# Optimization experiments

Hardware: AMD Instinct MI355X
Metric: run time of the kernel (lower is better)

## Reference

```python
import jax, jax.numpy as jnp
import numpy as np

N = 2048   # graph nodes
K = 3      # Chebyshev order of LSTM cell graph conv
IN = 2     # input feature dim (in/out flow)
H = 64     # hidden dim
B = 16     # batch
T = 12     # encoder sequence length


def _cheb(L, x, order):
    """Chebyshev polynomial features. x: [B, N, F] -> [B, N, order*F]."""
    Tk = [x]
    if order > 1:
        Tk.append(jnp.einsum('nm,bmf->bnf', L, x))
    for _ in range(2, order):
        Tk.append(2.0 * jnp.einsum('nm,bmf->bnf', L, Tk[-1]) - Tk[-2])
    return jnp.concatenate(Tk, axis=-1)


def _cell(L, x, h, c, W, b):
    """Graph-conv LSTM cell. x: [B,N,IN], h/c: [B,N,H]."""
    comb = jnp.concatenate([x, h], axis=-1)          # [B, N, IN+H]
    gates = _cheb(L, comb, K) @ W + b                # [B, N, 4H]
    i, f, o, g = jnp.split(gates, 4, axis=-1)
    c2 = jax.nn.sigmoid(f) * c + jax.nn.sigmoid(i) * jnp.tanh(g)
    h2 = jax.nn.sigmoid(o) * jnp.tanh(c2)
    return h2, c2


def setup_inputs() -> dict:
    rng = np.random.default_rng(0)
    # random sparse symmetric adjacency (avg degree ~8) -> normalized Laplacian
    A = rng.random((N, N)) < 8.0 / N
    A = np.triu(A, 1)
    A = (A | A.T).astype(np.float32)
    d = np.clip(A.sum(1), 1.0, None)
    dinv = 1.0 / np.sqrt(d)
    Lap = (np.eye(N, dtype=np.float32) - dinv[:, None] * A * dinv[None, :]).astype(np.float32)

    key = jax.random.key(0)
    k1, k2, k3 = jax.random.split(key, 3)
    return {
        'input_tensor': jax.random.normal(k1, (B, T, N, IN), jnp.float32),
        'L': jnp.asarray(Lap),
        'W_cell': jax.random.normal(k2, (K * (IN + H), 4 * H), jnp.float32) * 0.05,
        'b_cell': jnp.zeros((4 * H,), jnp.float32),
        'W0': jax.random.normal(k3, (H, IN), jnp.float32) * 0.05,
        'b0': jnp.zeros((IN,), jnp.float32),
        'future': 12,
    }


def reference(input_tensor, L, W_cell, b_cell, W0, b0, future):
    bsz = input_tensor.shape[0]
    h0 = jnp.zeros((bsz, N, H), input_tensor.dtype)
    c0 = jnp.zeros((bsz, N, H), input_tensor.dtype)

    # encoder: unroll ConvLSTM over the input sequence
    def enc_step(carry, xt):
        h, c = carry
        h, c = _cell(L, xt, h, c, W_cell, b_cell)
        return (h, c), None

    (h, c), _ = jax.lax.scan(enc_step, (h0, c0), jnp.swapaxes(input_tensor, 0, 1))

    # conv0 has K=1 => per-node linear; first prediction from last hidden state
    x = jnp.tanh(h @ W0 + b0)                         # [B, N, IN]

    def dec_step(carry, _):
        h, c, x = carry
        h, c = _cell(L, x, h, c, W_cell, b_cell)
        x2 = jnp.tanh(h @ W0 + b0)
        return (h, c, x2), x2

    _, xs = jax.lax.scan(dec_step, (h, c, x), None, length=future - 1)
    if future > 1:
        out = jnp.concatenate([x[:, None], jnp.swapaxes(xs, 0, 1)], axis=1)
    else:
        out = x[:, None]
    return out  # [B, future, N, IN]
```

## Files before the change

### kernel.cpp

```cpp
#include <hip/hip_runtime.h>
#include <cstdint>
#include <cstddef>

#define NN   2048
#define BB   16
#define TT   12
#define FUT  12
#define HH   64
#define GG   256
#define KP   224
#define ELLW 72
#define ASTR 232
#define NODE_F 80

typedef __attribute__((ext_vector_type(8))) short bf16x8;
typedef __attribute__((ext_vector_type(4))) float f32x4;

__device__ __forceinline__ float sigmoidf_(float x) {
    return 1.f / (1.f + __expf(-x));
}
__device__ __forceinline__ float tanhf_(float x) {
    const float e = __expf(2.f * x);
    return 1.f - 2.f / (e + 1.f);
}
__device__ __forceinline__ unsigned short f2bf(float x) {
    unsigned u = __builtin_bit_cast(unsigned, x);
    u += 0x7fffu + ((u >> 16) & 1u);
    return (unsigned short)(u >> 16);
}
__device__ __forceinline__ float bf2f(unsigned short s) {
    unsigned u = ((unsigned)s) << 16;
    return __builtin_bit_cast(float, u);
}

__global__ __launch_bounds__(256) void build_ell(
    const float* __restrict__ L, int* __restrict__ cols,
    float* __restrict__ vals, int* __restrict__ cnt)
{
    const int n = blockIdx.x;
    const int t = threadIdx.x;
    const float* row = L + (size_t)n * NN;
    float v[8];
    int c = 0;
#pragma unroll
    for (int i = 0; i < 8; ++i) {
        v[i] = row[t * 8 + i];
        c += (v[i] != 0.f);
    }
    __shared__ int s[256];
    s[t] = c;
    __syncthreads();
    for (int d = 1; d < 256; d <<= 1) {
        int add = (t >= d) ? s[t - d] : 0;
        __syncthreads();
        s[t] += add;
        __syncthreads();
    }
    int o = s[t] - c;
#pragma unroll
    for (int i = 0; i < 8; ++i) {
        if (v[i] != 0.f) {
            if (o < ELLW) {
                cols[n * ELLW + o] = t * 8 + i;
                vals[n * ELLW + o] = v[i];
            }
            ++o;
        }
    }
    if (t == 255) {
        int cn = (s[255] < ELLW) ? s[255] : ELLW;
        int cn4 = (cn + 3) & ~3;
        if (cn4 > ELLW) cn4 = ELLW;
        for (int p = cn; p < cn4; ++p) {
            cols[n * ELLW + p] = n;
            vals[n * ELLW + p] = 0.f;
        }
        cnt[n] = cn4;
    }
}

__global__ __launch_bounds__(256) void wt_prep(
    const float* __restrict__ W, short* __restrict__ Wh, short* __restrict__ Wl)
{
    const int col = blockIdx.x;
    const int k = threadIdx.x;
    if (k < KP) {
        const float x = (k < 198) ? W[(size_t)k * GG + col] : 0.f;
        const unsigned short h = f2bf(x);
        const unsigned short l = f2bf(x - bf2f(h));
        Wh[(size_t)col * KP + k] = (short)h;
        Wl[(size_t)col * KP + k] = (short)l;
    }
}

__global__ __launch_bounds__(256) void x_trans(
    const float* __restrict__ input, float* __restrict__ xt)
{
    const int o = blockIdx.x * 256 + threadIdx.x;
    const int e = o & 1;
    const int b = (o >> 1) & 15;
    const int n = (o >> 5) & (NN - 1);
    const int t = o >> 16;
    xt[o] = input[(((size_t)b * TT + t) * NN + n) * 2 + e];
}

__global__ __launch_bounds__(256) void spmm_t1(
    const float* __restrict__ xt,
    const float* __restrict__ h,
    const int* __restrict__ cols, const float* __restrict__ vals,
    const int* __restrict__ cnt, float* __restrict__ t1)
{
    const int w = threadIdx.x >> 6, lane = threadIdx.x & 63;
    const int b = lane >> 2, j = lane & 3;
    const int n = blockIdx.x;
    const int cn = cnt[n];
    const int* cp = cols + n * ELLW;
    const float* vp = vals + n * ELLW;
    const int qoff = (4 * w + j) * 4;
    float a0 = 0.f, a1 = 0.f, a2 = 0.f, a3 = 0.f;
    float ax0 = 0.f, ax1 = 0.f;
#pragma unroll 4
    for (int jj = 0; jj < cn; ++jj) {
        const int m = cp[jj];
        const float v = vp[jj];
        const float4 g = *(const float4*)&h[((size_t)m * 16 + b) * HH + qoff];
        a0 += v * g.x; a1 += v * g.y; a2 += v * g.z; a3 += v * g.w;
        if (w == 0) {
            const float2 xg = *(const float2*)&xt[((size_t)m * 16 + b) * 2];
            ax0 += v * xg.x; ax1 += v * xg.y;
        }
    }
    float* o = t1 + ((size_t)n * 16 + b) * NODE_F;
    *(float4*)&o[qoff] = (float4){a0, a1, a2, a3};
    if (w == 0 && j == 0) {
        o[64] = ax0;
        o[65] = ax1;
    }
}

__global__ __launch_bounds__(256, 5) void cell_fused(
    const float* __restrict__ xt,
    float* __restrict__ h, float* __restrict__ c,
    const float* __restrict__ t1g,
    const int* __restrict__ cols, const float* __restrict__ vals,
    const int* __restrict__ cnt,
    const short* __restrict__ Wh, const short* __restrict__ Wl,
    const float* __restrict__ bc,
    const float* __restrict__ W0, const float* __restrict__ b0,
    float* __restrict__ xout,
    float* __restrict__ out, int jslot)
{
    __shared__ unsigned short Ah[32][ASTR];
    __shared__ unsigned short Al[32][ASTR];
    __shared__ float proj[4][32][2];
    const int tid = threadIdx.x, w = tid >> 6, lane = tid & 63;
    const int q = lane >> 4, c16 = lane & 15;
    const int b = lane >> 2, j = lane & 3;
    const int n0 = blockIdx.x * 2;
    const int qoff = (4 * w + j) * 4;

    auto put = [&](int r, int k, float v) {
        const unsigned short hi = f2bf(v);
        Ah[r][k] = hi;
        Al[r][k] = f2bf(v - bf2f(hi));
    };

    {
        const int zr = tid >> 3, zs = tid & 7;
#pragma unroll
        for (int k0 = 198; k0 < 232; k0 += 8) {
            const int k = k0 + zs;
            if (k < 232) { Ah[zr][k] = 0; Al[zr][k] = 0; }
        }
    }

#pragma unroll
    for (int ln = 0; ln < 2; ++ln) {
        const int n = n0 + ln;
        const size_t rb = (size_t)n * 16 + b;
        const int r = ln * 16 + b;
        const float4 hq = *(const float4*)&h[rb * HH + qoff];
        const float4 tq = *(const float4*)&t1g[rb * NODE_F + qoff];
        float xo0 = 0.f, xo1 = 0.f, t160 = 0.f, t161 = 0.f;
        if (w == 1) {
            const float2 xv = *(const float2*)&xt[rb * 2];
            xo0 = xv.x; xo1 = xv.y;
            const float2 tv = *(const float2*)&t1g[rb * NODE_F + 64];
            t160 = tv.x; t161 = tv.y;
        }
        const int cn = cnt[n];
        const int* cp = cols + n * ELLW;
        const float* vp = vals + n * ELLW;
        float a0 = 0.f, a1 = 0.f, a2 = 0.f, a3 = 0.f, ax0 = 0.f, ax1 = 0.f;
#pragma unroll 4
        for (int jj = 0; jj < cn; ++jj) {
            const int m = cp[jj];
            const float v = vp[jj];
            const size_t mb = ((size_t)m * 16 + b) * NODE_F;
            const float4 g = *(const float4*)&t1g[mb + qoff];
            a0 += v * g.x; a1 += v * g.y; a2 += v * g.z; a3 += v * g.w;
            if (w == 1) {
                const float2 gx = *(const float2*)&t1g[mb + 64];
                ax0 += v * gx.x; ax1 += v * gx.y;
            }
        }
        put(r, 2 + qoff + 0, hq.x);  put(r, 2 + qoff + 1, hq.y);
        put(r, 2 + qoff + 2, hq.z);  put(r, 2 + qoff + 3, hq.w);
        put(r, 68 + qoff + 0, tq.x); put(r, 68 + qoff + 1, tq.y);
        put(r, 68 + qoff + 2, tq.z); put(r, 68 + qoff + 3, tq.w);
        put(r, 134 + qoff + 0, 2.f * a0 - hq.x);
        put(r, 134 + qoff + 1, 2.f * a1 - hq.y);
        put(r, 134 + qoff + 2, 2.f * a2 - hq.z);
        put(r, 134 + qoff + 3, 2.f * a3 - hq.w);
        if (w == 1 && j == 0) {
            put(r, 0, xo0);  put(r, 1, xo1);
            put(r, 66, t160); put(r, 67, t161);
            put(r, 132, 2.f * ax0 - xo0);
            put(r, 133, 2.f * ax1 - xo1);
        }
    }
    __syncthreads();

    f32x4 acc[2][4];
#pragma unroll
    for (int rt = 0; rt < 2; ++rt)
#pragma unroll
        for (int g = 0; g < 4; ++g) acc[rt][g] = (f32x4){0.f, 0.f, 0.f, 0.f};

    const int wc = w;
#pragma unroll 1
    for (int kc = 0; kc < 7; ++kc) {
        const int ko = kc * 32 + q * 8;
        bf16x8 ah[2], al[2];
#pragma unroll
        for (int rt = 0; rt < 2; ++rt) {
            ah[rt] = *(const bf16x8*)&Ah[rt * 16 + c16][ko];
            al[rt] = *(const bf16x8*)&Al[rt * 16 + c16][ko];
        }
        bf16x8 bh[4], bl[4];
#pragma unroll
        for (int g = 0; g < 4; ++g) {
            const int col = (wc + 4 * g) * 16 + c16;
            const size_t wo = (size_t)col * KP + ko;
            bh[g] = *(const bf16x8*)(Wh + wo);
            bl[g] = *(const bf16x8*)(Wl + wo);
        }
#pragma unroll
        for (int rt = 0; rt < 2; ++rt)
#pragma unroll
            for (int g = 0; g < 4; ++g) {
                acc[rt][g] = __builtin_amdgcn_mfma_f32_16x16x32_bf16(ah[rt], bh[g], acc[rt][g], 0, 0, 0);
                acc[rt][g] = __builtin_amdgcn_mfma_f32_16x16x32_bf16(al[rt], bh[g], acc[rt][g], 0, 0, 0);
                acc[rt][g] = __builtin_amdgcn_mfma_f32_16x16x32_bf16(ah[rt], bl[g], acc[rt][g], 0, 0, 0);
            }
    }

    const int u = 16 * wc + c16;
    const float bi = bc[u], bfv = bc[64 + u], bo = bc[128 + u], bg = bc[192 + u];
    float h2v[2][4];
#pragma unroll
    for (int rt = 0; rt < 2; ++rt) {
        const int n = n0 + rt;
#pragma unroll
        for (int reg = 0; reg < 4; ++reg) {
            const int bb = q * 4 + reg;
            const size_t idx = ((size_t)n * 16 + bb) * HH + u;
            const float ig = sigmoidf_(acc[rt][0][reg] + bi);
            const float fg = sigmoidf_(acc[rt][1][reg] + bfv);
            const float og = sigmoidf_(acc[rt][2][reg] + bo);
            const float gg = tanhf_(acc[rt][3][reg] + bg);
            const float c2 = fg * c[idx] + ig * gg;
            const float h2 = og * tanhf_(c2);
            c[idx] = c2;
            h[idx] = h2;
            h2v[rt][reg] = h2;
        }
    }

    if (jslot >= 0) {
        const float w0u = W0[u * 2], w1u = W0[u * 2 + 1];
#pragma unroll
        for (int rt = 0; rt < 2; ++rt) {
#pragma unroll
            for (int reg = 0; reg < 4; ++reg) {
                float s0 = h2v[rt][reg] * w0u;
                float s1 = h2v[rt][reg] * w1u;
#pragma unroll
                for (int d = 1; d <= 8; d <<= 1) {
                    s0 += __shfl_xor(s0, d, 64);
                    s1 += __shfl_xor(s1, d, 64);
                }
                if (c16 == 0) {
                    const int lr = rt * 16 + q * 4 + reg;
                    proj[wc][lr][0] = s0;
                    proj[wc][lr][1] = s1;
                }
            }
        }
        __syncthreads();
        if (tid < 64) {
            const int lr = tid >> 1, comp = tid & 1;
            const float v = proj[0][lr][comp] + proj[1][lr][comp] +
                            proj[2][lr][comp] + proj[3][lr][comp] + b0[comp];
            const float y = tanhf_(v);
            const int n = n0 + (lr >> 4);
            const int bb = lr & 15;
            xout[((size_t)n * 16 + bb) * 2 + comp] = y;
            out[(((size_t)bb * FUT + jslot) * NN + n) * 2 + comp] = y;
        }
    }
}

extern "C" void kernel_launch(void* const* d_in, const int* in_sizes, int n_in,
                              void* d_out, int out_size, void* d_ws, size_t ws_size,
                              hipStream_t stream)
{
    const float* input = (const float*)d_in[0];
    const float* L     = (const float*)d_in[1];
    const float* W     = (const float*)d_in[2];
    const float* bc    = (const float*)d_in[3];
    const float* W0    = (const float*)d_in[4];
    const float* b0    = (const float*)d_in[5];

    char* ws = (char*)d_ws;
    size_t off = 0;
    auto carve = [&](size_t bytes) {
        void* p = ws + off;
        off += (bytes + 255) & ~(size_t)255;
        return p;
    };
    int*   cols  = (int*)  carve((size_t)NN * ELLW * 4);
    float* vals  = (float*)carve((size_t)NN * ELLW * 4);
    int*   cnt   = (int*)  carve((size_t)NN * 4);
    float* t1    = (float*)carve((size_t)NN * 16 * NODE_F * 4);
    float* h     = (float*)carve((size_t)NN * 16 * HH * 4);
    float* c     = (float*)carve((size_t)NN * 16 * HH * 4);
    float* xbuf  = (float*)carve((size_t)NN * 16 * 2 * 4);
    float* xtall = (float*)carve((size_t)TT * NN * 16 * 2 * 4);
    short* Wh    = (short*)carve((size_t)GG * KP * 2);
    short* Wl    = (short*)carve((size_t)GG * KP * 2);
    float* out   = (float*)d_out;

    build_ell<<<NN, 256, 0, stream>>>(L, cols, vals, cnt);
    wt_prep<<<GG, 256, 0, stream>>>(W, Wh, Wl);
    x_trans<<<(TT * NN * 16 * 2) / 256, 256, 0, stream>>>(input, xtall);
    hipMemsetAsync(h, 0, (size_t)NN * 16 * HH * 4, stream);
    hipMemsetAsync(c, 0, (size_t)NN * 16 * HH * 4, stream);

    for (int t = 0; t < TT; ++t) {
        const float* xt = xtall + (size_t)t * NN * 16 * 2;
        spmm_t1<<<NN, 256, 0, stream>>>(xt, h, cols, vals, cnt, t1);
        cell_fused<<<NN / 2, 256, 0, stream>>>(xt, h, c, t1, cols, vals, cnt,
                                               Wh, Wl, bc, W0, b0, xbuf, out,
                                               (t == TT - 1) ? 0 : -1);
    }
    for (int jstep = 1; jstep < FUT; ++jstep) {
        spmm_t1<<<NN, 256, 0, stream>>>(xbuf, h, cols, vals, cnt, t1);
        cell_fused<<<NN / 2, 256, 0, stream>>>(xbuf, h, c, t1, cols, vals, cnt,
                                               Wh, Wl, bc, W0, b0, xbuf, out, jstep);
    }
}
```

Measured before the change: 1.260 ms.

## Split Chebyshev T1 buffer into h/x arrays and process one node per block

The first-order Chebyshev term is now stored as a dense 64-wide hidden array plus a separate 2-wide input array, replacing the padded 80-float interleaved rows. This aligns the neighbour gathers. The fused cell kernel now handles a single node per block, with half the LDS and accumulators and a higher occupancy hint, and launches twice as many blocks. In exchange, each block reloads the full split-bf16 weight tile for only 16 rows, which doubles weight fetch traffic through the caches.

```diff
diff --git a/kernel.cpp b/kernel.cpp
--- a/kernel.cpp
+++ b/kernel.cpp
@@ -11,7 +11,6 @@
 #define KP   224
 #define ELLW 72
 #define ASTR 232
-#define NODE_F 80
 
 typedef __attribute__((ext_vector_type(8))) short bf16x8;
 typedef __attribute__((ext_vector_type(4))) float f32x4;
@@ -108,7 +107,8 @@
     const float* __restrict__ xt,
     const float* __restrict__ h,
     const int* __restrict__ cols, const float* __restrict__ vals,
-    const int* __restrict__ cnt, float* __restrict__ t1)
+    const int* __restrict__ cnt,
+    float* __restrict__ t1h, float* __restrict__ t1x)
 {
     const int w = threadIdx.x >> 6, lane = threadIdx.x & 63;
     const int b = lane >> 2, j = lane & 3;
@@ -130,18 +130,18 @@
             ax0 += v * xg.x; ax1 += v * xg.y;
         }
     }
-    float* o = t1 + ((size_t)n * 16 + b) * NODE_F;
-    *(float4*)&o[qoff] = (float4){a0, a1, a2, a3};
+    *(float4*)&t1h[((size_t)n * 16 + b) * HH + qoff] = (float4){a0, a1, a2, a3};
     if (w == 0 && j == 0) {
-        o[64] = ax0;
-        o[65] = ax1;
-    }
-}
-
-__global__ __launch_bounds__(256, 5) void cell_fused(
+        t1x[((size_t)n * 16 + b) * 2]     = ax0;
+        t1x[((size_t)n * 16 + b) * 2 + 1] = ax1;
+    }
+}
+
+__global__ __launch_bounds__(256, 8) void cell_fused(
     const float* __restrict__ xt,
     float* __restrict__ h, float* __restrict__ c,
-    const float* __restrict__ t1g,
+    const float* __restrict__ t1h,
+    const float* __restrict__ t1x,
     const int* __restrict__ cols, const float* __restrict__ vals,
     const int* __restrict__ cnt,
     const short* __restrict__ Wh, const short* __restrict__ Wl,
@@ -150,13 +150,13 @@
     float* __restrict__ xout,
     float* __restrict__ out, int jslot)
 {
-    __shared__ unsigned short Ah[32][ASTR];
-    __shared__ unsigned short Al[32][ASTR];
-    __shared__ float proj[4][32][2];
+    __shared__ unsigned short Ah[16][ASTR];
+    __shared__ unsigned short Al[16][ASTR];
+    __shared__ float proj[4][16][2];
     const int tid = threadIdx.x, w = tid >> 6, lane = tid & 63;
     const int q = lane >> 4, c16 = lane & 15;
     const int b = lane >> 2, j = lane & 3;
-    const int n0 = blockIdx.x * 2;
+    const int n = blockIdx.x;
     const int qoff = (4 * w + j) * 4;
 
     auto put = [&](int r, int k, float v) {
@@ -166,26 +166,23 @@
     };
 
     {
-        const int zr = tid >> 3, zs = tid & 7;
-#pragma unroll
-        for (int k0 = 198; k0 < 232; k0 += 8) {
+        const int zr = tid >> 4, zs = tid & 15;
+#pragma unroll
+        for (int k0 = 198; k0 < 232; k0 += 16) {
             const int k = k0 + zs;
             if (k < 232) { Ah[zr][k] = 0; Al[zr][k] = 0; }
         }
     }
 
-#pragma unroll
-    for (int ln = 0; ln < 2; ++ln) {
-        const int n = n0 + ln;
+    {
         const size_t rb = (size_t)n * 16 + b;
-        const int r = ln * 16 + b;
         const float4 hq = *(const float4*)&h[rb * HH + qoff];
-        const float4 tq = *(const float4*)&t1g[rb * NODE_F + qoff];
+        const float4 tq = *(const float4*)&t1h[rb * HH + qoff];
         float xo0 = 0.f, xo1 = 0.f, t160 = 0.f, t161 = 0.f;
         if (w == 1) {
             const float2 xv = *(const float2*)&xt[rb * 2];
             xo0 = xv.x; xo1 = xv.y;
-            const float2 tv = *(const float2*)&t1g[rb * NODE_F + 64];
+            const float2 tv = *(const float2*)&t1x[rb * 2];
             t160 = tv.x; t161 = tv.y;
         }
         const int cn = cnt[n];
@@ -196,14 +193,15 @@
         for (int jj = 0; jj < cn; ++jj) {
             const int m = cp[jj];
             const float v = vp[jj];
-            const size_t mb = ((size_t)m * 16 + b) * NODE_F;
-            const float4 g = *(const float4*)&t1g[mb + qoff];
+            const size_t mb = (size_t)m * 16 + b;
+            const float4 g = *(const float4*)&t1h[mb * HH + qoff];
             a0 += v * g.x; a1 += v * g.y; a2 += v * g.z; a3 += v * g.w;
             if (w == 1) {
-                const float2 gx = *(const float2*)&t1g[mb + 64];
+                const float2 gx = *(const float2*)&t1x[mb * 2];
                 ax0 += v * gx.x; ax1 += v * gx.y;
             }
         }
+        const int r = b;
         put(r, 2 + qoff + 0, hq.x);  put(r, 2 + qoff + 1, hq.y);
         put(r, 2 + qoff + 2, hq.z);  put(r, 2 + qoff + 3, hq.w);
         put(r, 68 + qoff + 0, tq.x); put(r, 68 + qoff + 1, tq.y);
@@ -213,7 +211,7 @@
         put(r, 134 + qoff + 2, 2.f * a2 - hq.z);
         put(r, 134 + qoff + 3, 2.f * a3 - hq.w);
         if (w == 1 && j == 0) {
-            put(r, 0, xo0);  put(r, 1, xo1);
+            put(r, 0, xo0);   put(r, 1, xo1);
             put(r, 66, t160); put(r, 67, t161);
             put(r, 132, 2.f * ax0 - xo0);
             put(r, 133, 2.f * ax1 - xo1);
@@ -221,92 +219,75 @@
     }
     __syncthreads();
 
-    f32x4 acc[2][4];
-#pragma unroll
-    for (int rt = 0; rt < 2; ++rt)
-#pragma unroll
-        for (int g = 0; g < 4; ++g) acc[rt][g] = (f32x4){0.f, 0.f, 0.f, 0.f};
-
-    const int wc = w;
+    f32x4 acc[4];
+#pragma unroll
+    for (int g = 0; g < 4; ++g) acc[g] = (f32x4){0.f, 0.f, 0.f, 0.f};
+
 #pragma unroll 1
     for (int kc = 0; kc < 7; ++kc) {
         const int ko = kc * 32 + q * 8;
-        bf16x8 ah[2], al[2];
-#pragma unroll
-        for (int rt = 0; rt < 2; ++rt) {
-            ah[rt] = *(const bf16x8*)&Ah[rt * 16 + c16][ko];
-            al[rt] = *(const bf16x8*)&Al[rt * 16 + c16][ko];
-        }
-        bf16x8 bh[4], bl[4];
-#pragma unroll
-        for (int g = 0; g < 4; ++g) {
-            const int col = (wc + 4 * g) * 16 + c16;
-            const size_t wo = (size_t)col * KP + ko;
-            bh[g] = *(const bf16x8*)(Wh + wo);
-            bl[g] = *(const bf16x8*)(Wl + wo);
-        }
-#pragma unroll
-        for (int rt = 0; rt < 2; ++rt)
-#pragma unroll
-            for (int g = 0; g < 4; ++g) {
-                acc[rt][g] = __builtin_amdgcn_mfma_f32_16x16x32_bf16(ah[rt], bh[g], acc[rt][g], 0, 0, 0);
-                acc[rt][g] = __builtin_amdgcn_mfma_f32_16x16x32_bf16(al[rt], bh[g], acc[rt][g], 0, 0, 0);
-                acc[rt][g] = __builtin_amdgcn_mfma_f32_16x16x32_bf16(ah[rt], bl[g], acc[rt][g], 0, 0, 0);
-            }
-    }
-
-    const int u = 16 * wc + c16;
+        const bf16x8 ah = *(const bf16x8*)&Ah[c16][ko];
+        const bf16x8 al = *(const bf16x8*)&Al[c16][ko];
+#pragma unroll
+        for (int gp = 0; gp < 4; gp += 2) {
+            const int col0 = (w + 4 * gp) * 16 + c16;
+            const int col1 = (w + 4 * (gp + 1)) * 16 + c16;
+            const bf16x8 bh0 = *(const bf16x8*)(Wh + (size_t)col0 * KP + ko);
+            const bf16x8 bl0 = *(const bf16x8*)(Wl + (size_t)col0 * KP + ko);
+            const bf16x8 bh1 = *(const bf16x8*)(Wh + (size_t)col1 * KP + ko);
+            const bf16x8 bl1 = *(const bf16x8*)(Wl + (size_t)col1 * KP + ko);
+            acc[gp] = __builtin_amdgcn_mfma_f32_16x16x32_bf16(ah, bh0, acc[gp], 0, 0, 0);
+            acc[gp] = __builtin_amdgcn_mfma_f32_16x16x32_bf16(al, bh0, acc[gp], 0, 0, 0);
+            acc[gp] = __builtin_amdgcn_mfma_f32_16x16x32_bf16(ah, bl0, acc[gp], 0, 0, 0);
+            acc[gp + 1] = __builtin_amdgcn_mfma_f32_16x16x32_bf16(ah, bh1, acc[gp + 1], 0, 0, 0);
+            acc[gp + 1] = __builtin_amdgcn_mfma_f32_16x16x32_bf16(al, bh1, acc[gp + 1], 0, 0, 0);
+            acc[gp + 1] = __builtin_amdgcn_mfma_f32_16x16x32_bf16(ah, bl1, acc[gp + 1], 0, 0, 0);
+        }
+    }
+
+    const int u = 16 * w + c16;
     const float bi = bc[u], bfv = bc[64 + u], bo = bc[128 + u], bg = bc[192 + u];
-    float h2v[2][4];
-#pragma unroll
-    for (int rt = 0; rt < 2; ++rt) {
-        const int n = n0 + rt;
-#pragma unroll
-        for (int reg = 0; reg < 4; ++reg) {
-            const int bb = q * 4 + reg;
-            const size_t idx = ((size_t)n * 16 + bb) * HH + u;
-            const float ig = sigmoidf_(acc[rt][0][reg] + bi);
-            const float fg = sigmoidf_(acc[rt][1][reg] + bfv);
-            const float og = sigmoidf_(acc[rt][2][reg] + bo);
-            const float gg = tanhf_(acc[rt][3][reg] + bg);
-            const float c2 = fg * c[idx] + ig * gg;
-            const float h2 = og * tanhf_(c2);
-            c[idx] = c2;
-            h[idx] = h2;
-            h2v[rt][reg] = h2;
-        }
+    float h2v[4];
+#pragma unroll
+    for (int reg = 0; reg < 4; ++reg) {
+        const int bb = q * 4 + reg;
+        const size_t idx = ((size_t)n * 16 + bb) * HH + u;
+        const float ig = sigmoidf_(acc[0][reg] + bi);
+        const float fg = sigmoidf_(acc[1][reg] + bfv);
+        const float og = sigmoidf_(acc[2][reg] + bo);
+        const float gg = tanhf_(acc[3][reg] + bg);
+        const float c2 = fg * c[idx] + ig * gg;
+        const float h2 = og * tanhf_(c2);
+        c[idx] = c2;
+        h[idx] = h2;
+        h2v[reg] = h2;
     }
 
     if (jslot >= 0) {
         const float w0u = W0[u * 2], w1u = W0[u * 2 + 1];
 #pragma unroll
-        for (int rt = 0; rt < 2; ++rt) {
-#pragma unroll
-            for (int reg = 0; reg < 4; ++reg) {
-                float s0 = h2v[rt][reg] * w0u;
-                float s1 = h2v[rt][reg] * w1u;
-#pragma unroll
-                for (int d = 1; d <= 8; d <<= 1) {
-                    s0 += __shfl_xor(s0, d, 64);
-                    s1 += __shfl_xor(s1, d, 64);
-                }
-                if (c16 == 0) {
-                    const int lr = rt * 16 + q * 4 + reg;
-                    proj[wc][lr][0] = s0;
-                    proj[wc][lr][1] = s1;
-                }
+        for (int reg = 0; reg < 4; ++reg) {
+            float s0 = h2v[reg] * w0u;
+            float s1 = h2v[reg] * w1u;
+#pragma unroll
+            for (int d = 1; d <= 8; d <<= 1) {
+                s0 += __shfl_xor(s0, d, 64);
+                s1 += __shfl_xor(s1, d, 64);
             }
+            if (c16 == 0) {
+                const int lr = q * 4 + reg;
+                proj[w][lr][0] = s0;
+                proj[w][lr][1] = s1;
+            }
         }
         __syncthreads();
-        if (tid < 64) {
+        if (tid < 32) {
             const int lr = tid >> 1, comp = tid & 1;
             const float v = proj[0][lr][comp] + proj[1][lr][comp] +
                             proj[2][lr][comp] + proj[3][lr][comp] + b0[comp];
             const float y = tanhf_(v);
-            const int n = n0 + (lr >> 4);
-            const int bb = lr & 15;
-            xout[((size_t)n * 16 + bb) * 2 + comp] = y;
-            out[(((size_t)bb * FUT + jslot) * NN + n) * 2 + comp] = y;
+            xout[((size_t)n * 16 + lr) * 2 + comp] = y;
+            out[(((size_t)lr * FUT + jslot) * NN + n) * 2 + comp] = y;
         }
     }
 }
@@ -332,7 +313,8 @@
     int*   cols  = (int*)  carve((size_t)NN * ELLW * 4);
     float* vals  = (float*)carve((size_t)NN * ELLW * 4);
     int*   cnt   = (int*)  carve((size_t)NN * 4);
-    float* t1    = (float*)carve((size_t)NN * 16 * NODE_F * 4);
+    float* t1h   = (float*)carve((size_t)NN * 16 * HH * 4);
+    float* t1x   = (float*)carve((size_t)NN * 16 * 2 * 4);
     float* h     = (float*)carve((size_t)NN * 16 * HH * 4);
     float* c     = (float*)carve((size_t)NN * 16 * HH * 4);
     float* xbuf  = (float*)carve((size_t)NN * 16 * 2 * 4);
@@ -349,14 +331,14 @@
 
     for (int t = 0; t < TT; ++t) {
         const float* xt = xtall + (size_t)t * NN * 16 * 2;
-        spmm_t1<<<NN, 256, 0, stream>>>(xt, h, cols, vals, cnt, t1);
-        cell_fused<<<NN / 2, 256, 0, stream>>>(xt, h, c, t1, cols, vals, cnt,
-                                               Wh, Wl, bc, W0, b0, xbuf, out,
-                                               (t == TT - 1) ? 0 : -1);
+        spmm_t1<<<NN, 256, 0, stream>>>(xt, h, cols, vals, cnt, t1h, t1x);
+        cell_fused<<<NN, 256, 0, stream>>>(xt, h, c, t1h, t1x, cols, vals, cnt,
+                                           Wh, Wl, bc, W0, b0, xbuf, out,
+                                           (t == TT - 1) ? 0 : -1);
     }
     for (int jstep = 1; jstep < FUT; ++jstep) {
-        spmm_t1<<<NN, 256, 0, stream>>>(xbuf, h, cols, vals, cnt, t1);
-        cell_fused<<<NN / 2, 256, 0, stream>>>(xbuf, h, c, t1, cols, vals, cnt,
-                                               Wh, Wl, bc, W0, b0, xbuf, out, jstep);
-    }
-}
+        spmm_t1<<<NN, 256, 0, stream>>>(xbuf, h, cols, vals, cnt, t1h, t1x);
+        cell_fused<<<NN, 256, 0, stream>>>(xbuf, h, c, t1h, t1x, cols, vals, cnt,
+                                           Wh, Wl, bc, W0, b0, xbuf, out, jstep);
+    }
+}
```

Measured after the change: 1.376 ms. 9.2% more time.
